# Kernel optimization log

Measured on AMD Instinct MI355X. Metric: run time of the kernel, lower is better.

The kernel has to match this reference:

```python
import jax, jax.numpy as jnp
import numpy as np

N_HEADS = 16

@jax.checkpoint
def feature_fn(x, neurons, weights):
    # x [B,S,D], neurons [N,D,R], weights [B,S,N] -> h [B,S,R]
    all_h = jnp.einsum('bsd,ndr->bsnr', x, neurons)
    return jnp.einsum('bsnr,bsn->bsr', all_h, weights)

@jax.checkpoint
def restore_fn(h, neurons, weights):
    # h [B,S,R], neurons [N,R,D], weights [B,S,N] -> out [B,S,D]
    all_out = jnp.einsum('bsr,nrd->bsnd', h, neurons)
    return jnp.einsum('bsnd,bsn->bsd', all_out, weights)


def setup_inputs() -> dict:
    key = jax.random.key(0)
    ks = jax.random.split(key, 12)
    B, S, D, R, N = 2, 2048, 1024, 128, 8
    inp = {
        'x': jax.random.normal(ks[0], (B, S, D), jnp.float32),
        'f_qk_neurons': jax.random.normal(ks[1], (N, D, R), jnp.float32) * 0.02,
        'f_v_neurons': jax.random.normal(ks[2], (N, D, R), jnp.float32) * 0.02,
        'r_qk_neurons': jax.random.normal(ks[3], (N, R, D), jnp.float32) * 0.02,
        'r_v_neurons': jax.random.normal(ks[4], (N, R, D), jnp.float32) * 0.02,
        'fqk_weights_Q': jax.random.uniform(ks[5], (B, S, N), jnp.float32),
        'fqk_weights_K': jax.random.uniform(ks[6], (B, S, N), jnp.float32),
        'fv_weights': jax.random.uniform(ks[7], (B, S, N), jnp.float32),
        'rqk_weights_Q': jax.random.uniform(ks[8], (B, S, N), jnp.float32),
        'rqk_weights_K': jax.random.uniform(ks[9], (B, S, N), jnp.float32),
        'rv_weights': jax.random.uniform(ks[10], (B, S, N), jnp.float32),
        'W_O': jax.random.normal(ks[11], (D, D), jnp.float32) * 0.02,
    }
    return inp


def reference(x, f_qk_neurons, f_v_neurons, r_qk_neurons, r_v_neurons,
              fqk_weights_Q, fqk_weights_K, fv_weights,
              rqk_weights_Q, rqk_weights_K, rv_weights, W_O):
    B, S, D = x.shape
    H = N_HEADS
    d_head = D // H
    # neuron-mixture feature projections (shared QK pool)
    h_q = feature_fn(x, f_qk_neurons, fqk_weights_Q)
    h_k = feature_fn(x, f_qk_neurons, fqk_weights_K)
    h_v = feature_fn(x, f_v_neurons, fv_weights)
    # neuron-mixture restore projections
    Q = restore_fn(h_q, r_qk_neurons, rqk_weights_Q)
    K = restore_fn(h_k, r_qk_neurons, rqk_weights_K)
    V = restore_fn(h_v, r_v_neurons, rv_weights)
    # split heads: [B,S,D] -> [B,H,S,d_head]
    Q = Q.reshape(B, S, H, d_head).transpose(0, 2, 1, 3)
    K = K.reshape(B, S, H, d_head).transpose(0, 2, 1, 3)
    V = V.reshape(B, S, H, d_head).transpose(0, 2, 1, 3)
    scale = jnp.sqrt(jnp.float32(d_head))
    scores = jnp.einsum('bhsd,bhtd->bhst', Q, K) / scale
    causal_mask = jnp.tril(jnp.ones((S, S), dtype=jnp.bool_))
    scores = jnp.where(causal_mask, scores, jnp.finfo(scores.dtype).min)
    attn = jax.nn.softmax(scores, axis=-1)
    attn_out = jnp.einsum('bhst,bhtd->bhsd', attn, V)
    attn_out = attn_out.transpose(0, 2, 1, 3).reshape(B, S, D)
    return attn_out @ W_O
```

## Files before the change

kernel.cpp:

```cpp
#include <hip/hip_runtime.h>
#include <stdint.h>

typedef __attribute__((ext_vector_type(8))) __bf16 bf16x8;
typedef __attribute__((ext_vector_type(4))) float f32x4;
typedef __attribute__((ext_vector_type(4))) unsigned short us4;
typedef __attribute__((ext_vector_type(8))) unsigned short us8v;

__device__ __forceinline__ unsigned short f2b(float f){
  unsigned int u = __builtin_bit_cast(unsigned int, f);
  unsigned int r = (u + 0x7fffu + ((u >> 16) & 1u)) >> 16;
  return (unsigned short)r;
}
__device__ __forceinline__ unsigned short f2b_fast(float f){
  unsigned int u = __builtin_bit_cast(unsigned int, f);
  return (unsigned short)((u + 0x8000u) >> 16);
}
__device__ __forceinline__ float b2f(unsigned short h){
  unsigned int u = ((unsigned int)h) << 16;
  return __builtin_bit_cast(float, u);
}

#define KDIM 1024

__global__ __launch_bounds__(256) void k_prep(
    const float* __restrict__ x,   unsigned short* __restrict__ Xbf,
    const float* __restrict__ fqk, unsigned short* __restrict__ FqkT,
    const float* __restrict__ fv,  unsigned short* __restrict__ FvT,
    const float* __restrict__ rqk, unsigned short* __restrict__ RqkT,
    const float* __restrict__ rv,  unsigned short* __restrict__ RvT,
    const float* __restrict__ wo,  unsigned short* __restrict__ WOT)
{
  __shared__ float tile[32][33];
  int blk = blockIdx.x;
  int tid = threadIdx.x;
  if (blk < 4096){
    int idx = blk * 256 + tid;
    float4 v = ((const float4*)x)[idx];
    us4 o; o.x = f2b(v.x); o.y = f2b(v.y); o.z = f2b(v.z); o.w = f2b(v.w);
    ((us4*)Xbf)[idx] = o;
    return;
  }
  int t = blk - 4096;
  int mid = t >> 10;
  int within = t & 1023;
  const float* src; unsigned short* dst;
  int b, R, C, tr, tc;
  if (mid < 2){
    src = mid == 0 ? fqk : fv;  dst = mid == 0 ? FqkT : FvT;
    R = 1024; C = 128;
    b = within >> 7; int tw = within & 127; tr = tw >> 2; tc = tw & 3;
  } else {
    src = mid == 2 ? rqk : (mid == 3 ? rv : wo);
    dst = mid == 2 ? RqkT : (mid == 3 ? RvT : WOT);
    R = 1024; C = 1024;
    b = 0; tr = within >> 5; tc = within & 31;
  }
  int r = tid >> 3, c0 = (tid & 7) * 4;
  size_t base = (size_t)b * R * C;
  float4 v = *(const float4*)&src[base + (size_t)(tr*32 + r) * C + tc*32 + c0];
  tile[r][c0+0] = v.x; tile[r][c0+1] = v.y; tile[r][c0+2] = v.z; tile[r][c0+3] = v.w;
  __syncthreads();
  us4 o;
  o.x = f2b(tile[c0+0][r]); o.y = f2b(tile[c0+1][r]);
  o.z = f2b(tile[c0+2][r]); o.w = f2b(tile[c0+3][r]);
  *(us4*)&dst[base + (size_t)(tc*32 + r) * R + tr*32 + c0] = o;
}

__global__ __launch_bounds__(256) void k_mix(const unsigned short* __restrict__ AH,
    const float* __restrict__ fwq, const float* __restrict__ fwk, const float* __restrict__ fwv,
    const float* __restrict__ rwq, const float* __restrict__ rwk, const float* __restrict__ rwv,
    unsigned short* __restrict__ gq, unsigned short* __restrict__ gk, unsigned short* __restrict__ gv){
  int tid = threadIdx.x;
  int lb = tid >> 5, rq = tid & 31;
  int bs = blockIdx.x * 8 + lb;
  const unsigned short* row = AH + (size_t)bs * 2048;
  float fq[8], fk[8], fv8[8], rqw[8], rkw[8], rvw[8];
  #pragma unroll
  for (int n = 0; n < 8; n++){
    fq[n] = fwq[bs*8+n]; fk[n] = fwk[bs*8+n]; fv8[n] = fwv[bs*8+n];
    rqw[n] = rwq[bs*8+n]; rkw[n] = rwk[bs*8+n]; rvw[n] = rwv[bs*8+n];
  }
  float hq[4] = {}, hk[4] = {}, hv[4] = {};
  #pragma unroll
  for (int n = 0; n < 8; n++){
    us4 a = *(const us4*)&row[n*128 + rq*4];
    us4 av = *(const us4*)&row[1024 + n*128 + rq*4];
    #pragma unroll
    for (int j = 0; j < 4; j++){
      float af = b2f(a[j]);
      hq[j] += af * fq[n]; hk[j] += af * fk[n];
      hv[j] += b2f(av[j]) * fv8[n];
    }
  }
  #pragma unroll
  for (int n = 0; n < 8; n++){
    us4 oq, ok, ov;
    #pragma unroll
    for (int j = 0; j < 4; j++){
      oq[j] = f2b(rqw[n] * hq[j]);
      ok[j] = f2b(rkw[n] * hk[j]);
      ov[j] = f2b(rvw[n] * hv[j]);
    }
    *(us4*)&gq[(size_t)bs*1024 + n*128 + rq*4] = oq;
    *(us4*)&gk[(size_t)bs*1024 + n*128 + rq*4] = ok;
    *(us4*)&gv[(size_t)bs*1024 + n*128 + rq*4] = ov;
  }
}

__global__ __launch_bounds__(256) void k_transpose_v(const unsigned short* __restrict__ Vp,
                                                     unsigned short* __restrict__ Vt){
  __shared__ unsigned short tile[32][36];
  int blk = blockIdx.x;
  int bh = blk >> 7, rem = blk & 127;
  int t = rem >> 3, tl = rem & 7, ts = tl >> 1, td = tl & 1;
  int tid = threadIdx.x;
  int r = tid >> 3, c0 = (tid & 7) * 4;
  us4 v = *(const us4*)&Vp[((size_t)(bh*2048 + t*128 + ts*32 + r)) * 64 + td*32 + c0];
  *(us4*)&tile[r][c0] = v;
  __syncthreads();
  us4 o;
  o.x = tile[c0+0][r]; o.y = tile[c0+1][r]; o.z = tile[c0+2][r]; o.w = tile[c0+3][r];
  *(us4*)&Vt[((size_t)((bh*16 + t)*64 + td*32 + r)) * 128 + ts*32 + c0] = o;
}


__device__ __forceinline__ void load_lds16(const void* g, void* l){
  __builtin_amdgcn_global_load_lds((const __attribute__((address_space(1))) unsigned int*)g,
                                   (__attribute__((address_space(3))) unsigned int*)l, 16, 0, 0);
}

template<int OUT_MODE, int BN, int ND, int NTILE>
__global__ __launch_bounds__(256) void k_gemm_bt3(
    const unsigned short* __restrict__ A0, const unsigned short* __restrict__ B0, void* __restrict__ C0,
    const unsigned short* __restrict__ A1, const unsigned short* __restrict__ B1, void* __restrict__ C1,
    const unsigned short* __restrict__ A2, const unsigned short* __restrict__ B2, void* __restrict__ C2)
{
  __shared__ unsigned short Al[2][128*32];
  __shared__ unsigned short Bl[2][BN*32];
  int nb8 = gridDim.x >> 3;
  int swz = (blockIdx.x & 7) * nb8 + (blockIdx.x >> 3);
  int job = swz / NTILE, bid = swz % NTILE;
  const unsigned short* A  = job == 0 ? A0 : (job == 1 ? A1 : A2);
  const unsigned short* Bt = job == 0 ? B0 : (job == 1 ? B1 : B2);
  void* C = job == 0 ? C0 : (job == 1 ? C1 : C2);
  constexpr int NBX = ND / BN;
  int bx = bid % NBX, by = bid / NBX;
  int m0 = by * 128, n0 = bx * BN;
  int tid = threadIdx.x, wid = tid >> 6, lane = tid & 63, l15 = lane & 15, g = lane >> 4;
  int wr = wid >> 1, wc = wid & 1;
  constexpr int WCN = BN / 2;
  constexpr int NACC = WCN / 16;

  auto stage = [&](int buf, int kt){
    #pragma unroll
    for (int i = 0; i < 2; i++){
      int c = i * 256 + tid;
      load_lds16(A + (size_t)(m0 + (c >> 2)) * KDIM + kt * 32 + (c & 3) * 8,
                 &Al[buf][(i * 256 + wid * 64) * 8]);
    }
    #pragma unroll
    for (int i = 0; i < BN/64; i++){
      int c = i * 256 + tid;
      load_lds16(Bt + (size_t)(n0 + (c >> 2)) * KDIM + kt * 32 + (c & 3) * 8,
                 &Bl[buf][(i * 256 + wid * 64) * 8]);
    }
  };

  f32x4 acc[4][NACC] = {};

  stage(0, 0);
  __syncthreads();
  int cur = 0;
  const int nk = KDIM / 32;
  for (int kt = 0; kt < nk; ++kt){
    if (kt + 1 < nk) stage(cur ^ 1, kt + 1);
    bf16x8 af[4], bfv[NACC];
    #pragma unroll
    for (int mi = 0; mi < 4; mi++)
      af[mi] = *(const bf16x8*)&Al[cur][(wr*64 + mi*16 + l15) * 32 + g * 8];
    #pragma unroll
    for (int ni = 0; ni < NACC; ni++)
      bfv[ni] = *(const bf16x8*)&Bl[cur][(wc*WCN + ni*16 + l15) * 32 + g * 8];
    #pragma unroll
    for (int mi = 0; mi < 4; mi++)
      #pragma unroll
      for (int ni = 0; ni < NACC; ni++)
        acc[mi][ni] = __builtin_amdgcn_mfma_f32_16x16x32_bf16(af[mi], bfv[ni], acc[mi][ni], 0, 0, 0);
    __syncthreads();
    cur ^= 1;
  }

  #pragma unroll
  for (int mi = 0; mi < 4; mi++){
    #pragma unroll
    for (int reg = 0; reg < 4; reg++){
      int row = m0 + wr*64 + mi*16 + g*4 + reg;
      #pragma unroll
      for (int ni = 0; ni < NACC; ni++){
        int col = n0 + wc*WCN + ni*16 + l15;
        float v = acc[mi][ni][reg];
        if (OUT_MODE == 0){
          ((float*)C)[(size_t)row * ND + col] = v;
        } else if (OUT_MODE == 1){
          ((unsigned short*)C)[(size_t)row * ND + col] = f2b(v);
        } else {
          int b = row >> 11, s = row & 2047, h = col >> 6, dh = col & 63;
          ((unsigned short*)C)[(((size_t)(b*16 + h)) * 2048 + s) * 64 + dh] = f2b(v);
        }
      }
    }
  }
}

#define PSTR 72
#define PBYTES 33792
__global__ __launch_bounds__(512) void k_attn(
    const unsigned short* __restrict__ Qp_, const unsigned short* __restrict__ Kp_,
    const unsigned short* __restrict__ Vt, unsigned short* __restrict__ AO,
    char* __restrict__ Pws)
{
  __shared__ unsigned short Klds[4096];
  __shared__ unsigned short Vlds[4096];
  __shared__ unsigned short Plds[8][32*PSTR];

  int xb = (blockIdx.x & 7) * 80 + (blockIdx.x >> 3);
  int bh = xb / 20;
  int slot = xb % 20;
  int qt = 0, s = slot;
  for (;;){ int ncq = (qt >> 1) + 1; if (s < ncq) break; s -= ncq; qt++; }
  int c = s;
  int nc = (qt >> 1) + 1;
  int b = bh >> 4, h = bh & 15;
  int q0 = qt * 256;
  int kv_lo = c * 512;
  int kv_hi = min((c + 1) * 512, q0 + 256);
  int niter = (kv_hi - kv_lo) >> 6;

  int tid = threadIdx.x, w = tid >> 6, lane = tid & 63, l15 = lane & 15, g = lane >> 4;
  const unsigned short* Qw = Qp_ + ((size_t)bh * 2048 + q0 + w*32) * 64;
  const unsigned short* Kb = Kp_ + (size_t)bh * 2048 * 64;
  const unsigned short* Vb = Vt + (size_t)bh * 16 * 64 * 128;
  unsigned short* Pw = &Plds[w][0];

  int srow = tid >> 3, sj = tid & 7;

  bf16x8 aq[2][2];
  #pragma unroll
  for (int m = 0; m < 2; m++)
    #pragma unroll
    for (int kk = 0; kk < 2; kk++)
      aq[m][kk] = *(const bf16x8*)(Qw + (m*16 + l15)*64 + kk*32 + g*8);

  const float cs = 0.125f;
  float l_run[2][4] = {};
  f32x4 acc_o[2][4] = {};

  us8v kA, vA, kB, vB;

  auto issue = [&](us8v& k0, us8v& v0, int kv0){
    k0 = *(const us8v*)(Kb + ((size_t)(kv0 + srow)) * 64 + sj*8);
    int t128 = kv0 >> 7, koff = kv0 & 64;
    v0 = *(const us8v*)(Vb + ((size_t)(t128*64 + srow)) * 128 + koff + sj*8);
  };
  auto put = [&](us8v k0, us8v v0){
    *(us8v*)&Klds[(sj*64 + srow)*8] = k0;
    *(us8v*)&Vlds[(sj*64 + srow)*8] = v0;
  };
  auto compute = [&](int kv0){
    f32x4 s4[2][4] = {};
    __builtin_amdgcn_s_setprio(1);
    #pragma unroll
    for (int ti = 0; ti < 4; ti++){
      #pragma unroll
      for (int kk = 0; kk < 2; kk++){
        bf16x8 kf = *(const bf16x8*)&Klds[((kk*4 + g)*64 + ti*16 + l15)*8];
        s4[0][ti] = __builtin_amdgcn_mfma_f32_16x16x32_bf16(aq[0][kk], kf, s4[0][ti], 0, 0, 0);
        s4[1][ti] = __builtin_amdgcn_mfma_f32_16x16x32_bf16(aq[1][kk], kf, s4[1][ti], 0, 0, 0);
      }
    }
    __builtin_amdgcn_s_setprio(0);
    bool partial = (kv0 + 64 > q0);
    #pragma unroll
    for (int m = 0; m < 2; m++){
      #pragma unroll
      for (int reg = 0; reg < 4; reg++){
        int row = q0 + w*32 + m*16 + g*4 + reg;
        #pragma unroll
        for (int ti = 0; ti < 4; ti++){
          float x = s4[m][ti][reg] * cs;
          if (partial){
            int col = kv0 + ti*16 + l15;
            if (col > row) x = -1e30f;
          }
          float p = __expf(x);
          l_run[m][reg] += p;
          Pw[(m*16 + g*4 + reg)*PSTR + ((ti ^ g)*16) + l15] = f2b_fast(p);
        }
      }
    }
    bf16x8 pa[2][2];
    #pragma unroll
    for (int m = 0; m < 2; m++)
      #pragma unroll
      for (int cc = 0; cc < 2; cc++){
        int tiL = cc*2 + (g >> 1);
        int tiS = tiL ^ ((l15 >> 2) & 3);
        pa[m][cc] = *(const bf16x8*)&Pw[(m*16 + l15)*PSTR + tiS*16 + (g & 1)*8];
      }
    __builtin_amdgcn_s_setprio(1);
    #pragma unroll
    for (int ni = 0; ni < 4; ni++){
      #pragma unroll
      for (int cc = 0; cc < 2; cc++){
        bf16x8 vf = *(const bf16x8*)&Vlds[((cc*4 + g)*64 + ni*16 + l15)*8];
        acc_o[0][ni] = __builtin_amdgcn_mfma_f32_16x16x32_bf16(pa[0][cc], vf, acc_o[0][ni], 0, 0, 0);
        acc_o[1][ni] = __builtin_amdgcn_mfma_f32_16x16x32_bf16(pa[1][cc], vf, acc_o[1][ni], 0, 0, 0);
      }
    }
    __builtin_amdgcn_s_setprio(0);
  };

  issue(kA, vA, kv_lo);
  put(kA, vA);
  __syncthreads();
  int it = 0;
  while (true){
    bool more = (it + 1 < niter);
    if (more) issue(kB, vB, kv_lo + (it+1)*64);
    compute(kv_lo + it*64);
    ++it;
    if (!more) break;
    __syncthreads();
    put(kB, vB);
    __syncthreads();

    more = (it + 1 < niter);
    if (more) issue(kA, vA, kv_lo + (it+1)*64);
    compute(kv_lo + it*64);
    ++it;
    if (!more) break;
    __syncthreads();
    put(kA, vA);
    __syncthreads();
  }

  #pragma unroll
  for (int m = 0; m < 2; m++)
    #pragma unroll
    for (int reg = 0; reg < 4; reg++){
      #pragma unroll
      for (int off = 1; off < 16; off <<= 1) l_run[m][reg] += __shfl_xor(l_run[m][reg], off);
    }

  if (nc == 1){
    #pragma unroll
    for (int m = 0; m < 2; m++)
      #pragma unroll
      for (int ni = 0; ni < 4; ni++)
        #pragma unroll
        for (int reg = 0; reg < 4; reg++){
          int row = q0 + w*32 + m*16 + g*4 + reg;
          int dh = ni*16 + l15;
          AO[((size_t)(b*2048 + row)) * 1024 + h*64 + dh] = f2b(acc_o[m][ni][reg] / l_run[m][reg]);
        }
  } else {
    int poff = 0;
    for (int q = 2; q < qt; ++q) poff += (q >> 1) + 1;
    char* P0 = Pws + ((size_t)(bh*18 + poff + c)) * PBYTES;
    unsigned short* Ob = (unsigned short*)P0;
    float* lb = (float*)(P0 + 32768);
    #pragma unroll
    for (int m = 0; m < 2; m++)
      #pragma unroll
      for (int ni = 0; ni < 4; ni++)
        #pragma unroll
        for (int reg = 0; reg < 4; reg++){
          int lrow = w*32 + m*16 + g*4 + reg;
          Ob[lrow*64 + ni*16 + l15] = f2b(acc_o[m][ni][reg]);
        }
    if (l15 == 0){
      #pragma unroll
      for (int m = 0; m < 2; m++)
        #pragma unroll
        for (int reg = 0; reg < 4; reg++){
          int lrow = w*32 + m*16 + g*4 + reg;
          lb[lrow] = l_run[m][reg];
        }
    }
  }
}

__global__ __launch_bounds__(256) void k_attn_reduce(const char* __restrict__ Pws,
                                                     unsigned short* __restrict__ AO){
  int blk = blockIdx.x;
  int rg = blk & 3, tmp = blk >> 2;
  int qq = tmp % 6, bh = tmp / 6;
  int qt = qq + 2;
  int b = bh >> 4, h = bh & 15;
  int nc = (qt >> 1) + 1;
  int poff = 0;
  for (int q = 2; q < qt; ++q) poff += (q >> 1) + 1;
  const char* base = Pws + ((size_t)(bh*18 + poff)) * PBYTES;
  int tid = threadIdx.x;
  int lrow = rg*64 + (tid >> 2);
  int d0 = (tid & 3) * 16;
  float o[16] = {};
  float l = 0.f;
  for (int cc = 0; cc < nc; ++cc){
    const unsigned short* Oc = (const unsigned short*)(base + (size_t)cc*PBYTES);
    const float* lc = (const float*)(base + (size_t)cc*PBYTES + 32768);
    us8v v0 = *(const us8v*)&Oc[lrow*64 + d0];
    us8v v1 = *(const us8v*)&Oc[lrow*64 + d0 + 8];
    #pragma unroll
    for (int j = 0; j < 8; j++){ o[j] += b2f(v0[j]); o[8+j] += b2f(v1[j]); }
    l += lc[lrow];
  }
  float inv = 1.f / l;
  us8v w0, w1;
  #pragma unroll
  for (int j = 0; j < 8; j++){ w0[j] = f2b(o[j]*inv); w1[j] = f2b(o[8+j]*inv); }
  size_t orow = ((size_t)(b*2048 + qt*256 + lrow)) * 1024 + h*64 + d0;
  *(us8v*)&AO[orow] = w0;
  *(us8v*)&AO[orow + 8] = w1;
}


extern "C" void kernel_launch(void* const* d_in, const int* in_sizes, int n_in,
                              void* d_out, int out_size, void* d_ws, size_t ws_size,
                              hipStream_t stream){
  const float* x    = (const float*)d_in[0];
  const float* fqk  = (const float*)d_in[1];
  const float* fv   = (const float*)d_in[2];
  const float* rqk  = (const float*)d_in[3];
  const float* rv   = (const float*)d_in[4];
  const float* fwQ  = (const float*)d_in[5];
  const float* fwK  = (const float*)d_in[6];
  const float* fwV  = (const float*)d_in[7];
  const float* rwQ  = (const float*)d_in[8];
  const float* rwK  = (const float*)d_in[9];
  const float* rwV  = (const float*)d_in[10];
  const float* wo   = (const float*)d_in[11];
  float* out = (float*)d_out;

  char* ws = (char*)d_ws;
  size_t off = 0;
  auto alloc = [&](size_t bytes)->void*{
    void* p = ws + off; off += (bytes + 255) & ~(size_t)255; return p;
  };
  unsigned short* FqkT = (unsigned short*)alloc(1024ull*1024*2);
  unsigned short* FvT  = (unsigned short*)alloc(1024ull*1024*2);
  unsigned short* RqkT = (unsigned short*)alloc(1024ull*1024*2);
  unsigned short* RvT  = (unsigned short*)alloc(1024ull*1024*2);
  unsigned short* WOT  = (unsigned short*)alloc(1024ull*1024*2);
  char* overlay = ws + off;
  unsigned short* Xbf  = (unsigned short*)alloc(4096ull*1024*2);
  unsigned short* AHc  = (unsigned short*)alloc(4096ull*2048*2);
  unsigned short* Gq   = (unsigned short*)alloc(4096ull*1024*2);
  unsigned short* Gk   = (unsigned short*)alloc(4096ull*1024*2);
  unsigned short* Gv   = (unsigned short*)alloc(4096ull*1024*2);
  unsigned short* Qp   = (unsigned short*)alloc(4096ull*1024*2);
  unsigned short* Kp   = (unsigned short*)alloc(4096ull*1024*2);
  unsigned short* Vpk  = (unsigned short*)alloc(4096ull*1024*2);
  unsigned short* Vtl  = (unsigned short*)alloc(32ull*16*64*128*2);
  unsigned short* AOm  = (unsigned short*)alloc(4096ull*1024*2);
  char* Pws = overlay;

  k_prep<<<9216, 256, 0, stream>>>(x, Xbf, fqk, FqkT, fv, FvT, rqk, RqkT, rv, RvT, wo, WOT);

  k_gemm_bt3<1,128,2048,512><<<512, 256, 0, stream>>>(Xbf, FqkT, AHc,
                                                      nullptr, nullptr, nullptr,
                                                      nullptr, nullptr, nullptr);
  k_mix<<<512, 256, 0, stream>>>(AHc, fwQ, fwK, fwV, rwQ, rwK, rwV, Gq, Gk, Gv);
  k_gemm_bt3<2,128,1024,256><<<768, 256, 0, stream>>>(Gq, RqkT, Qp, Gk, RqkT, Kp, Gv, RvT, Vpk);
  k_transpose_v<<<4096, 256, 0, stream>>>(Vpk, Vtl);
  k_attn<<<640, 512, 0, stream>>>(Qp, Kp, Vtl, AOm, Pws);
  k_attn_reduce<<<768, 256, 0, stream>>>(Pws, AOm);
  k_gemm_bt3<0,64,1024,512><<<512, 256, 0, stream>>>(AOm, WOT, out,
                                                     nullptr, nullptr, nullptr,
                                                     nullptr, nullptr, nullptr);
}
```

Before: 183.9 us.

## Stage GEMM epilogue through LDS, double-buffer attention K/V, rebalance KV splits

The bf16 GEMM epilogues now write accumulators into shared memory and then store 16-byte vectors to global memory, replacing scattered 2-byte stores. The attention kernel double-buffers its K/V LDS tiles, which removes one barrier per iteration. It also changes the KV split-K chunk from 512 to 768, giving fewer blocks (480) and fewer partials to reduce (640 reduce blocks). The trade-offs are extra LDS use, an added barrier in the epilogue, and coarser work units that may balance less well across CUs.

```diff
diff --git a/kernel.cpp b/kernel.cpp
--- a/kernel.cpp
+++ b/kernel.cpp
@@ -135,8 +135,9 @@
     const unsigned short* __restrict__ A1, const unsigned short* __restrict__ B1, void* __restrict__ C1,
     const unsigned short* __restrict__ A2, const unsigned short* __restrict__ B2, void* __restrict__ C2)
 {
-  __shared__ unsigned short Al[2][128*32];
-  __shared__ unsigned short Bl[2][BN*32];
+  __shared__ unsigned short Sh[2*128*32 + 2*BN*32];
+  unsigned short (*Al)[128*32] = (unsigned short(*)[128*32])Sh;
+  unsigned short (*Bl)[BN*32]  = (unsigned short(*)[BN*32])(Sh + 2*128*32);
   int nb8 = gridDim.x >> 3;
   int swz = (blockIdx.x & 7) * nb8 + (blockIdx.x >> 3);
   int job = swz / NTILE, bid = swz % NTILE;
@@ -190,23 +191,42 @@
     cur ^= 1;
   }
 
-  #pragma unroll
-  for (int mi = 0; mi < 4; mi++){
-    #pragma unroll
-    for (int reg = 0; reg < 4; reg++){
-      int row = m0 + wr*64 + mi*16 + g*4 + reg;
-      #pragma unroll
-      for (int ni = 0; ni < NACC; ni++){
-        int col = n0 + wc*WCN + ni*16 + l15;
-        float v = acc[mi][ni][reg];
-        if (OUT_MODE == 0){
-          ((float*)C)[(size_t)row * ND + col] = v;
-        } else if (OUT_MODE == 1){
-          ((unsigned short*)C)[(size_t)row * ND + col] = f2b(v);
-        } else {
-          int b = row >> 11, s = row & 2047, h = col >> 6, dh = col & 63;
-          ((unsigned short*)C)[(((size_t)(b*16 + h)) * 2048 + s) * 64 + dh] = f2b(v);
+  if constexpr (OUT_MODE == 0){
+    #pragma unroll
+    for (int mi = 0; mi < 4; mi++)
+      #pragma unroll
+      for (int reg = 0; reg < 4; reg++){
+        int row = m0 + wr*64 + mi*16 + g*4 + reg;
+        #pragma unroll
+        for (int ni = 0; ni < NACC; ni++){
+          int col = n0 + wc*WCN + ni*16 + l15;
+          ((float*)C)[(size_t)row * ND + col] = acc[mi][ni][reg];
         }
+      }
+  } else {
+    unsigned short* Cl = Sh;
+    #pragma unroll
+    for (int mi = 0; mi < 4; mi++)
+      #pragma unroll
+      for (int reg = 0; reg < 4; reg++){
+        int lrow = wr*64 + mi*16 + g*4 + reg;
+        #pragma unroll
+        for (int ni = 0; ni < NACC; ni++)
+          Cl[lrow*BN + wc*WCN + ni*16 + l15] = f2b(acc[mi][ni][reg]);
+      }
+    __syncthreads();
+    constexpr int VPT = (128*BN/8) / 256;
+    #pragma unroll
+    for (int i = 0; i < VPT; i++){
+      int idx = i*256 + tid;
+      int lrow = idx / (BN/8), c8 = (idx % (BN/8)) * 8;
+      us8v v = *(const us8v*)&Cl[lrow*BN + c8];
+      int row = m0 + lrow, col = n0 + c8;
+      if (OUT_MODE == 1){
+        *(us8v*)&((unsigned short*)C)[(size_t)row * ND + col] = v;
+      } else {
+        int b = row >> 11, s = row & 2047, h = col >> 6, dh = col & 63;
+        *(us8v*)&((unsigned short*)C)[(((size_t)(b*16 + h)) * 2048 + s) * 64 + dh] = v;
       }
     }
   }
@@ -219,21 +239,22 @@
     const unsigned short* __restrict__ Vt, unsigned short* __restrict__ AO,
     char* __restrict__ Pws)
 {
-  __shared__ unsigned short Klds[4096];
-  __shared__ unsigned short Vlds[4096];
+  __shared__ unsigned short Klds[2][4096];
+  __shared__ unsigned short Vlds[2][4096];
   __shared__ unsigned short Plds[8][32*PSTR];
 
-  int xb = (blockIdx.x & 7) * 80 + (blockIdx.x >> 3);
-  int bh = xb / 20;
-  int slot = xb % 20;
-  int qt = 0, s = slot;
-  for (;;){ int ncq = (qt >> 1) + 1; if (s < ncq) break; s -= ncq; qt++; }
-  int c = s;
-  int nc = (qt >> 1) + 1;
+  int xb = (blockIdx.x & 7) * 60 + (blockIdx.x >> 3);
+  int bh = xb / 15;
+  int slot = xb % 15;
+  int qt, c;
+  if (slot < 3){ qt = slot; c = 0; }
+  else if (slot < 9){ int s = slot - 3; qt = 3 + (s >> 1); c = s & 1; }
+  else { int s = slot - 9; qt = 6 + (s >= 3 ? 1 : 0); c = (s >= 3) ? s - 3 : s; }
+  int nc = qt < 3 ? 1 : (qt < 6 ? 2 : 3);
   int b = bh >> 4, h = bh & 15;
   int q0 = qt * 256;
-  int kv_lo = c * 512;
-  int kv_hi = min((c + 1) * 512, q0 + 256);
+  int kv_lo = c * 768;
+  int kv_hi = min((c + 1) * 768, q0 + 256);
   int niter = (kv_hi - kv_lo) >> 6;
 
   int tid = threadIdx.x, w = tid >> 6, lane = tid & 63, l15 = lane & 15, g = lane >> 4;
@@ -262,18 +283,18 @@
     int t128 = kv0 >> 7, koff = kv0 & 64;
     v0 = *(const us8v*)(Vb + ((size_t)(t128*64 + srow)) * 128 + koff + sj*8);
   };
-  auto put = [&](us8v k0, us8v v0){
-    *(us8v*)&Klds[(sj*64 + srow)*8] = k0;
-    *(us8v*)&Vlds[(sj*64 + srow)*8] = v0;
+  auto put = [&](int buf, us8v k0, us8v v0){
+    *(us8v*)&Klds[buf][(sj*64 + srow)*8] = k0;
+    *(us8v*)&Vlds[buf][(sj*64 + srow)*8] = v0;
   };
-  auto compute = [&](int kv0){
+  auto compute = [&](int buf, int kv0){
     f32x4 s4[2][4] = {};
     __builtin_amdgcn_s_setprio(1);
     #pragma unroll
     for (int ti = 0; ti < 4; ti++){
       #pragma unroll
       for (int kk = 0; kk < 2; kk++){
-        bf16x8 kf = *(const bf16x8*)&Klds[((kk*4 + g)*64 + ti*16 + l15)*8];
+        bf16x8 kf = *(const bf16x8*)&Klds[buf][((kk*4 + g)*64 + ti*16 + l15)*8];
         s4[0][ti] = __builtin_amdgcn_mfma_f32_16x16x32_bf16(aq[0][kk], kf, s4[0][ti], 0, 0, 0);
         s4[1][ti] = __builtin_amdgcn_mfma_f32_16x16x32_bf16(aq[1][kk], kf, s4[1][ti], 0, 0, 0);
       }
@@ -312,7 +333,7 @@
     for (int ni = 0; ni < 4; ni++){
       #pragma unroll
       for (int cc = 0; cc < 2; cc++){
-        bf16x8 vf = *(const bf16x8*)&Vlds[((cc*4 + g)*64 + ni*16 + l15)*8];
+        bf16x8 vf = *(const bf16x8*)&Vlds[buf][((cc*4 + g)*64 + ni*16 + l15)*8];
         acc_o[0][ni] = __builtin_amdgcn_mfma_f32_16x16x32_bf16(pa[0][cc], vf, acc_o[0][ni], 0, 0, 0);
         acc_o[1][ni] = __builtin_amdgcn_mfma_f32_16x16x32_bf16(pa[1][cc], vf, acc_o[1][ni], 0, 0, 0);
       }
@@ -321,27 +342,22 @@
   };
 
   issue(kA, vA, kv_lo);
-  put(kA, vA);
+  put(0, kA, vA);
   __syncthreads();
-  int it = 0;
+  int it = 0, cur = 0;
   while (true){
-    bool more = (it + 1 < niter);
-    if (more) issue(kB, vB, kv_lo + (it+1)*64);
-    compute(kv_lo + it*64);
-    ++it;
-    if (!more) break;
+    if (it + 1 < niter) issue(kB, vB, kv_lo + (it+1)*64);
+    compute(cur, kv_lo + it*64);
+    if (it + 1 < niter) put(cur ^ 1, kB, vB);
     __syncthreads();
-    put(kB, vB);
+    cur ^= 1; ++it;
+    if (it >= niter) break;
+    if (it + 1 < niter) issue(kA, vA, kv_lo + (it+1)*64);
+    compute(cur, kv_lo + it*64);
+    if (it + 1 < niter) put(cur ^ 1, kA, vA);
     __syncthreads();
-
-    more = (it + 1 < niter);
-    if (more) issue(kA, vA, kv_lo + (it+1)*64);
-    compute(kv_lo + it*64);
-    ++it;
-    if (!more) break;
-    __syncthreads();
-    put(kA, vA);
-    __syncthreads();
+    cur ^= 1; ++it;
+    if (it >= niter) break;
   }
 
   #pragma unroll
@@ -364,9 +380,8 @@
           AO[((size_t)(b*2048 + row)) * 1024 + h*64 + dh] = f2b(acc_o[m][ni][reg] / l_run[m][reg]);
         }
   } else {
-    int poff = 0;
-    for (int q = 2; q < qt; ++q) poff += (q >> 1) + 1;
-    char* P0 = Pws + ((size_t)(bh*18 + poff + c)) * PBYTES;
+    int poff = (qt < 6) ? (qt - 3) * 2 : 6 + (qt - 6) * 3;
+    char* P0 = Pws + ((size_t)(bh*12 + poff + c)) * PBYTES;
     unsigned short* Ob = (unsigned short*)P0;
     float* lb = (float*)(P0 + 32768);
     #pragma unroll
@@ -394,13 +409,12 @@
                                                      unsigned short* __restrict__ AO){
   int blk = blockIdx.x;
   int rg = blk & 3, tmp = blk >> 2;
-  int qq = tmp % 6, bh = tmp / 6;
-  int qt = qq + 2;
+  int qtp = tmp % 5, bh = tmp / 5;
+  int qt = qtp + 3;
   int b = bh >> 4, h = bh & 15;
-  int nc = (qt >> 1) + 1;
-  int poff = 0;
-  for (int q = 2; q < qt; ++q) poff += (q >> 1) + 1;
-  const char* base = Pws + ((size_t)(bh*18 + poff)) * PBYTES;
+  int nc = (qt < 6) ? 2 : 3;
+  int poff = (qt < 6) ? (qt - 3) * 2 : 6 + (qt - 6) * 3;
+  const char* base = Pws + ((size_t)(bh*12 + poff)) * PBYTES;
   int tid = threadIdx.x;
   int lrow = rg*64 + (tid >> 2);
   int d0 = (tid & 3) * 16;
@@ -473,8 +487,8 @@
   k_mix<<<512, 256, 0, stream>>>(AHc, fwQ, fwK, fwV, rwQ, rwK, rwV, Gq, Gk, Gv);
   k_gemm_bt3<2,128,1024,256><<<768, 256, 0, stream>>>(Gq, RqkT, Qp, Gk, RqkT, Kp, Gv, RvT, Vpk);
   k_transpose_v<<<4096, 256, 0, stream>>>(Vpk, Vtl);
-  k_attn<<<640, 512, 0, stream>>>(Qp, Kp, Vtl, AOm, Pws);
-  k_attn_reduce<<<768, 256, 0, stream>>>(Pws, AOm);
+  k_attn<<<480, 512, 0, stream>>>(Qp, Kp, Vtl, AOm, Pws);
+  k_attn_reduce<<<640, 256, 0, stream>>>(Pws, AOm);
   k_gemm_bt3<0,64,1024,512><<<512, 256, 0, stream>>>(AOm, WOT, out,
                                                      nullptr, nullptr, nullptr,
                                                      nullptr, nullptr, nullptr);
```

Result: faster. 175.5 us (-4.6%).
